# Performance work log

Hardware: AMD Instinct MI355X
Metric: run time of the kernel (lower is better)

The kernel has to match this reference:

```python
import jax, jax.numpy as jnp
import numpy as np

EPS = 1e-5


def spline_conv(x, src, dst, pseudo, W, root, bias, num_nodes, K=5):
    """Degree-1 open B-spline conv (torch_spline_conv semantics), mean aggregation.
    W: [kernel_total, Cin, Cout]. kernel_total==1 means trivial basis (kernel_size=1)."""
    E = src.shape[0]
    Cin = x.shape[1]
    KT = W.shape[0]
    x_j = x[src]                                            # [E, Cin] edge gather
    deg = jax.ops.segment_sum(jnp.ones((E,), x.dtype), dst, num_segments=num_nodes)
    deg = jnp.maximum(deg, 1.0)
    if KT == 1:
        agg = jax.ops.segment_sum(x_j, dst, num_segments=num_nodes)
        out = (agg / deg[:, None]) @ W[0]
    else:
        v = pseudo * (K - 1)                                # open spline: v in [0, K-1]
        f = jnp.clip(jnp.floor(v), 0.0, K - 2)
        frac = v - f                                        # [E, 2]
        fi = f.astype(jnp.int32)
        # bucket basis-weighted source features by (kernel_index, dst) then one dense einsum
        h = jnp.zeros((KT * num_nodes, Cin), x.dtype)
        for s0 in (0, 1):
            for s1 in (0, 1):
                b0 = frac[:, 0] if s0 else 1.0 - frac[:, 0]
                b1 = frac[:, 1] if s1 else 1.0 - frac[:, 1]
                basis = b0 * b1                             # [E]
                wi = (fi[:, 0] + s0) + K * (fi[:, 1] + s1)  # [E] kernel index in [0,25)
                seg = wi * num_nodes + dst
                h = h + jax.ops.segment_sum(basis[:, None] * x_j, seg,
                                            num_segments=KT * num_nodes)
        agg = jnp.einsum('knc,kco->no', h.reshape(KT, num_nodes, Cin), W)
        out = agg / deg[:, None]
    return out + x @ root + bias


def batch_norm(x, gamma, beta):
    m = x.mean(axis=0)
    var = jnp.mean((x - m) ** 2, axis=0)
    return gamma * (x - m) * jax.lax.rsqrt(var + EPS) + beta


def setup_inputs() -> dict:
    key = jax.random.key(0)
    ks = jax.random.split(key, 8)
    N, E, Cin, Cout = 50000, 800000, 32, 64
    x = jax.random.normal(ks[0], (N, Cin), jnp.float32)
    edge_index = jax.random.randint(ks[1], (2, E), 0, N, jnp.int32)
    edge_attr = jax.random.uniform(ks[2], (E, 2), jnp.float32)
    s = 0.1
    return {
        'x': x, 'edge_index': edge_index, 'edge_attr': edge_attr,
        'w1': jax.random.normal(ks[3], (25, Cin, Cout), jnp.float32) * s,
        'r1': jax.random.normal(ks[4], (Cin, Cout), jnp.float32) * s,
        'b1': jnp.zeros((Cout,), jnp.float32),
        'g1': jnp.ones((Cout,), jnp.float32),
        'beta1': jnp.zeros((Cout,), jnp.float32),
        'w2': jax.random.normal(ks[5], (25, Cout, Cout), jnp.float32) * s,
        'r2': jax.random.normal(ks[6], (Cout, Cout), jnp.float32) * s,
        'b2': jnp.zeros((Cout,), jnp.float32),
        'g2': jnp.ones((Cout,), jnp.float32),
        'beta2': jnp.zeros((Cout,), jnp.float32),
        'ws': jax.random.normal(ks[7], (1, Cin, Cout), jnp.float32) * s,
        'rs': jax.random.normal(jax.random.fold_in(key, 99), (Cin, Cout), jnp.float32) * s,
        'bs': jnp.zeros((Cout,), jnp.float32),
        'gs': jnp.ones((Cout,), jnp.float32),
        'betas': jnp.zeros((Cout,), jnp.float32),
    }


def reference(x, edge_index, edge_attr, w1, r1, b1, g1, beta1,
              w2, r2, b2, g2, beta2, ws, rs, bs, gs, betas):
    N = x.shape[0]
    src, dst = edge_index[0], edge_index[1]
    h = jax.nn.elu(batch_norm(spline_conv(x, src, dst, edge_attr, w1, r1, b1, N), g1, beta1))
    left = batch_norm(spline_conv(h, src, dst, edge_attr, w2, r2, b2, N), g2, beta2)
    short = batch_norm(spline_conv(x, src, dst, edge_attr, ws, rs, bs, N), gs, betas)
    return jax.nn.elu(left + short)
```

## Files before the change

kernel.cpp:

```cpp
#include <hip/hip_runtime.h>

#define NN 50000
#define NE 800000

typedef __attribute__((ext_vector_type(8))) short bf16x8;
typedef __attribute__((ext_vector_type(4))) float f32x4;
typedef __attribute__((ext_vector_type(2))) float f32x2;

__device__ __forceinline__ unsigned short f2bf(float f) {
    union { float f; unsigned u; } v; v.f = f;
    unsigned r = v.u + 0x7FFFu + ((v.u >> 16) & 1u);
    return (unsigned short)(r >> 16);
}

__device__ __forceinline__ int4 ld_ep(const int4* ep, unsigned idx) {
    return *(const int4*)((const char*)ep + (size_t)(idx * 16u));
}
__device__ __forceinline__ float ld_x(const float* X, unsigned byteoff) {
    return *(const float*)((const char*)X + (size_t)byteoff);
}

__device__ __forceinline__ int us_idx(int kk, int r, int m) {
    return kk*544 + (r >> 3)*136 + m*8 + (r & 7);
}

template<bool HS>
__device__ __forceinline__ void edge_acc(float* h, float& hs, const int4& p, float x) {
    const f32x2 zero = {0.f, 0.f};
    f32x2 vp = {__int_as_float(p.z), __int_as_float(p.w)};
    f32x2 wxy[5];
#pragma unroll
    for (int r = 0; r < 5; ++r) {
        f32x2 wr = 1.f - __builtin_elementwise_abs(vp - (float)r);
        wxy[r] = __builtin_elementwise_max(wr, zero);
    }
    if (HS) hs += x;
#pragma unroll
    for (int r1 = 0; r1 < 5; ++r1) {
        float ty = x * wxy[r1].y;
#pragma unroll
        for (int r0 = 0; r0 < 5; ++r0)
            h[r1*5 + r0] = fmaf(wxy[r0].x, ty, h[r1*5 + r0]);
    }
}

__global__ __launch_bounds__(256) void k_zero(int* degi, int* cur, float* stats) {
    int i = blockIdx.x*256 + threadIdx.x;
    int stride = gridDim.x*256;
    for (int j = i; j < NN; j += stride) { degi[j] = 0; cur[j] = 0; }
    if (i < 384) stats[i] = 0.f;
}

__global__ __launch_bounds__(256) void k_hist(const int* __restrict__ dst, int* degi) {
    int e = blockIdx.x*256 + threadIdx.x;
    if (e < NE) atomicAdd(&degi[dst[e]], 1);
}

__global__ __launch_bounds__(256) void k_scan_block(const int* __restrict__ degi,
                                                    int* off, int* bsum) {
    __shared__ int sh[256];
    int t = threadIdx.x;
    int base = blockIdx.x * 1024;
    int v[4]; int s = 0;
#pragma unroll
    for (int j = 0; j < 4; j++) {
        int idx = base + t*4 + j;
        v[j] = (idx < NN) ? degi[idx] : 0;
        s += v[j];
    }
    sh[t] = s; __syncthreads();
    for (int ofs = 1; ofs < 256; ofs <<= 1) {
        int x = (t >= ofs) ? sh[t - ofs] : 0;
        __syncthreads();
        sh[t] += x;
        __syncthreads();
    }
    int ex = sh[t] - s;
#pragma unroll
    for (int j = 0; j < 4; j++) {
        int idx = base + t*4 + j;
        if (idx < NN) off[idx] = ex;
        ex += v[j];
    }
    if (t == 255) bsum[blockIdx.x] = sh[255];
}

__global__ __launch_bounds__(256) void k_scan_top(const int* __restrict__ bsum,
                                                  int* bpre, int nb) {
    __shared__ int sh[256];
    int t = threadIdx.x;
    int s = (t < nb) ? bsum[t] : 0;
    sh[t] = s; __syncthreads();
    for (int ofs = 1; ofs < 256; ofs <<= 1) {
        int x = (t >= ofs) ? sh[t - ofs] : 0;
        __syncthreads();
        sh[t] += x;
        __syncthreads();
    }
    if (t < nb) bpre[t] = sh[t] - s;
}

__global__ __launch_bounds__(256) void k_scan_add(int* off, const int* __restrict__ bpre) {
    int i = blockIdx.x*256 + threadIdx.x;
    if (i < NN) off[i] += bpre[i >> 10];
    if (i == 0) off[NN] = NE;
}

__global__ __launch_bounds__(256) void k_scatter(const int* __restrict__ src,
                                                 const int* __restrict__ dst,
                                                 const float* __restrict__ ea,
                                                 const int* __restrict__ off, int* cur,
                                                 int4* __restrict__ ep) {
    int e = blockIdx.x*256 + threadIdx.x;
    if (e >= NE) return;
    int d = dst[e];
    int p = off[d] + atomicAdd(&cur[d], 1);
    float v0 = ea[2*e]     * 4.f;
    float v1 = ea[2*e + 1] * 4.f;
    ep[p] = make_int4(src[e], 0, __float_as_int(v0), __float_as_int(v1));
}

__global__ __launch_bounds__(256) void k_wprep(const float* __restrict__ W,
                                               const float* __restrict__ root,
                                               int KTC, unsigned short* Wb) {
    int tid = blockIdx.x*256 + threadIdx.x;
    int lane = tid & 63, cot = (tid >> 6) & 3, kk = tid >> 8;
    int co = 16*cot + (lane & 15);
    int kbase = kk*32 + ((lane >> 4) * 8);
    union { unsigned short s[8]; uint4 v; } u;
#pragma unroll
    for (int j = 0; j < 8; j++) {
        int k = kbase + j;
        float val = (k < KTC) ? W[(size_t)k*64 + co] : root[(size_t)(k - KTC)*64 + co];
        u.s[j] = f2bf(val);
    }
    *(uint4*)(Wb + (size_t)tid * 8) = u.v;
}

__global__ __launch_bounds__(512, 4) void k_conv1s(
        const float* __restrict__ X,
        const int* __restrict__ off,
        const int4* __restrict__ ep,
        const unsigned short* __restrict__ Wb1,
        const unsigned short* __restrict__ WbS,
        const float* __restrict__ b1,
        const float* __restrict__ bs,
        float* __restrict__ agg1,
        float* __restrict__ aggS) {
    __shared__ __align__(16) unsigned short hb[28*544];
    const int t = threadIdx.x;
    const int g = t >> 5;
    const int ci = t & 31;
    const int n0 = blockIdx.x * 16;
    const int n = n0 + g;

    float h[25], hs = 0.f;
#pragma unroll
    for (int i = 0; i < 25; ++i) h[i] = 0.f;

    const int ebeg = off[n], eend = off[n + 1];
    const int last = eend - 1;
    const float rdeg = 1.f / (float)max(eend - ebeg, 1);

    for (int i = ebeg; i < eend; i += 4) {
        int4 p[4]; float xv[4];
#pragma unroll
        for (int u = 0; u < 4; ++u) p[u] = ld_ep(ep, (unsigned)min(i + u, last));
#pragma unroll
        for (int u = 0; u < 4; ++u) {
            xv[u] = ld_x(X, (unsigned)p[u].x * 128u + (unsigned)ci * 4u);
            if (i + u >= eend) xv[u] = 0.f;
        }
#pragma unroll
        for (int u = 0; u < 4; ++u) edge_acc<true>(h, hs, p[u], xv[u]);
    }

    const int bw = us_idx(0, ci, g);
    const unsigned short xbf = f2bf(X[(size_t)n*32 + ci]);
#pragma unroll
    for (int wi = 0; wi < 25; ++wi) hb[wi*544 + bw] = f2bf(h[wi] * rdeg);
    hb[25*544 + bw] = xbf;
    hb[26*544 + bw] = f2bf(hs * rdeg);
    hb[27*544 + bw] = xbf;
    __syncthreads();

    const int lane = t & 63, w = t >> 6;
    const int m = lane & 15, qq = lane >> 4;
    const int co = (w & 3)*16 + m;
    if (w < 4) {
        f32x4 acc = {0.f, 0.f, 0.f, 0.f};
        for (int kk = 0; kk < 26; ++kk) {
            bf16x8 av = *(const bf16x8*)&hb[kk*544 + qq*136 + m*8];
            bf16x8 bv = *(const bf16x8*)(Wb1 + (size_t)((kk*4 + w)*64 + lane) * 8);
            acc = __builtin_amdgcn_mfma_f32_16x16x32_bf16(av, bv, acc, 0, 0, 0);
        }
        const float bb = b1[co];
#pragma unroll
        for (int r = 0; r < 4; ++r)
            agg1[(size_t)(n0 + qq*4 + r)*64 + co] = acc[r] + bb;
    } else {
        f32x4 accs = {0.f, 0.f, 0.f, 0.f};
#pragma unroll
        for (int s = 0; s < 2; ++s) {
            bf16x8 av = *(const bf16x8*)&hb[(26 + s)*544 + qq*136 + m*8];
            bf16x8 bv = *(const bf16x8*)(WbS + (size_t)((s*4 + (w & 3))*64 + lane) * 8);
            accs = __builtin_amdgcn_mfma_f32_16x16x32_bf16(av, bv, accs, 0, 0, 0);
        }
        const float bb = bs[co];
#pragma unroll
        for (int r = 0; r < 4; ++r)
            aggS[(size_t)(n0 + qq*4 + r)*64 + co] = accs[r] + bb;
    }
}

__global__ __launch_bounds__(512, 4) void k_conv2(
        const float* __restrict__ X,
        const int* __restrict__ off,
        const int4* __restrict__ ep,
        const unsigned short* __restrict__ Wb2,
        const float* __restrict__ b2,
        float* __restrict__ agg) {
    __shared__ __align__(16) unsigned short hb[52*544];
    const int t = threadIdx.x, lane = t & 63, w = t >> 6;
    const int n0 = blockIdx.x * 16;
    const int kh = lane >> 5, r = lane & 31;

#pragma unroll
    for (int nn = 0; nn < 2; ++nn) {
        const int g = 2*w + nn;
        const int n = n0 + g;
        float h[25];
#pragma unroll
        for (int i = 0; i < 25; ++i) h[i] = 0.f;
        float hsd = 0.f;

        const int ebeg = off[n], eend = off[n + 1];
        const int last = eend - 1;
        const float rdeg = 1.f / (float)max(eend - ebeg, 1);

        for (int i = ebeg; i < eend; i += 4) {
            int4 p[4]; float xv[4];
#pragma unroll
            for (int u = 0; u < 4; ++u) p[u] = ld_ep(ep, (unsigned)min(i + u, last));
#pragma unroll
            for (int u = 0; u < 4; ++u) {
                xv[u] = ld_x(X, (unsigned)p[u].x * 256u + (unsigned)lane * 4u);
                if (i + u >= eend) xv[u] = 0.f;
            }
#pragma unroll
            for (int u = 0; u < 4; ++u) edge_acc<false>(h, hsd, p[u], xv[u]);
        }

        const int bw = us_idx(0, r, g);
#pragma unroll
        for (int wi = 0; wi < 25; ++wi)
            hb[(wi*2 + kh)*544 + bw] = f2bf(h[wi] * rdeg);
        hb[(50 + kh)*544 + bw] = f2bf(X[(size_t)n*64 + lane]);
    }
    __syncthreads();

    if (w >= 4) return;

    const int m = lane & 15, qq = lane >> 4;
    f32x4 acc = {0.f, 0.f, 0.f, 0.f};
    for (int kk = 0; kk < 52; ++kk) {
        bf16x8 av = *(const bf16x8*)&hb[kk*544 + qq*136 + m*8];
        bf16x8 bv = *(const bf16x8*)(Wb2 + (size_t)((kk*4 + w)*64 + lane) * 8);
        acc = __builtin_amdgcn_mfma_f32_16x16x32_bf16(av, bv, acc, 0, 0, 0);
    }
    const int co = w*16 + m;
    const float bb = b2[co];
#pragma unroll
    for (int rr = 0; rr < 4; ++rr)
        agg[(size_t)(n0 + qq*4 + rr)*64 + co] = acc[rr] + bb;
}

__global__ __launch_bounds__(256) void k_bnstats(const float* __restrict__ agg, float* stats) {
    __shared__ float sh0[256], sh1[256];
    int t = threadIdx.x;
    float s = 0.f, ss = 0.f;
    int stride = gridDim.x * 256;
    for (int i = blockIdx.x*256 + t; i < NN*64; i += stride) {
        float v = agg[i];
        s += v; ss += v*v;
    }
    sh0[t] = s; sh1[t] = ss;
    __syncthreads();
    if (t < 64) {
        float a = sh0[t] + sh0[t+64] + sh0[t+128] + sh0[t+192];
        float b = sh1[t] + sh1[t+64] + sh1[t+128] + sh1[t+192];
        atomicAdd(&stats[t], a);
        atomicAdd(&stats[64 + t], b);
    }
}

__device__ __forceinline__ float eluf(float u) { return u > 0.f ? u : expm1f(u); }

__global__ __launch_bounds__(256) void k_bn_elu(const float* __restrict__ agg,
                                                const float* __restrict__ stats,
                                                const float* __restrict__ gamma,
                                                const float* __restrict__ beta,
                                                float* __restrict__ out) {
    int i = blockIdx.x*256 + threadIdx.x;
    if (i >= NN*16) return;
    float4 v = ((const float4*)agg)[i];
    float r[4] = {v.x, v.y, v.z, v.w};
    int c0 = (i << 2) & 63;
#pragma unroll
    for (int j = 0; j < 4; j++) {
        int c = c0 + j;
        float mu = stats[c] * (1.f/NN);
        float var = stats[64 + c] * (1.f/NN) - mu*mu;
        float sc = gamma[c] * rsqrtf(fmaxf(var, 0.f) + 1e-5f);
        r[j] = eluf((r[j] - mu)*sc + beta[c]);
    }
    ((float4*)out)[i] = make_float4(r[0], r[1], r[2], r[3]);
}

__global__ __launch_bounds__(256) void k_bn_final(const float* __restrict__ a2,
                                                  const float* __restrict__ st2,
                                                  const float* __restrict__ g2,
                                                  const float* __restrict__ be2,
                                                  const float* __restrict__ as,
                                                  const float* __restrict__ sts,
                                                  const float* __restrict__ gs,
                                                  const float* __restrict__ bes,
                                                  float* __restrict__ out) {
    int i = blockIdx.x*256 + threadIdx.x;
    if (i >= NN*16) return;
    float4 v2 = ((const float4*)a2)[i];
    float4 vs = ((const float4*)as)[i];
    float r2v[4] = {v2.x, v2.y, v2.z, v2.w};
    float rsv[4] = {vs.x, vs.y, vs.z, vs.w};
    float o[4];
    int c0 = (i << 2) & 63;
#pragma unroll
    for (int j = 0; j < 4; j++) {
        int c = c0 + j;
        float mu2 = st2[c] * (1.f/NN);
        float var2 = st2[64 + c] * (1.f/NN) - mu2*mu2;
        float sc2 = g2[c] * rsqrtf(fmaxf(var2, 0.f) + 1e-5f);
        float mus = sts[c] * (1.f/NN);
        float vars = sts[64 + c] * (1.f/NN) - mus*mus;
        float scs = gs[c] * rsqrtf(fmaxf(vars, 0.f) + 1e-5f);
        float u = (r2v[j] - mu2)*sc2 + be2[c] + (rsv[j] - mus)*scs + bes[c];
        o[j] = eluf(u);
    }
    ((float4*)out)[i] = make_float4(o[0], o[1], o[2], o[3]);
}

extern "C" void kernel_launch(void* const* d_in, const int* in_sizes, int n_in,
                              void* d_out, int out_size, void* d_ws, size_t ws_size,
                              hipStream_t stream) {
    const float* x   = (const float*)d_in[0];
    const int*   ei  = (const int*)d_in[1];
    const float* ea  = (const float*)d_in[2];
    const float* w1  = (const float*)d_in[3];
    const float* r1  = (const float*)d_in[4];
    const float* b1  = (const float*)d_in[5];
    const float* g1  = (const float*)d_in[6];
    const float* be1 = (const float*)d_in[7];
    const float* w2  = (const float*)d_in[8];
    const float* r2  = (const float*)d_in[9];
    const float* b2  = (const float*)d_in[10];
    const float* g2  = (const float*)d_in[11];
    const float* be2 = (const float*)d_in[12];
    const float* wsN = (const float*)d_in[13];
    const float* rs  = (const float*)d_in[14];
    const float* bs  = (const float*)d_in[15];
    const float* gs  = (const float*)d_in[16];
    const float* bes = (const float*)d_in[17];
    const int* srcp = ei;
    const int* dstp = ei + NE;

    char* wsb = (char*)d_ws;
    size_t o = 0;
    auto alloc = [&](size_t bytes) -> char* {
        char* p = wsb + o;
        o += (bytes + 255) & ~(size_t)255;
        return p;
    };
    int*    degi    = (int*)   alloc((size_t)NN * 4);
    int*    cur     = (int*)   alloc((size_t)NN * 4);
    int*    off     = (int*)   alloc((size_t)(NN + 1) * 4);
    int*    bsum    = (int*)   alloc(256 * 4);
    int*    bpre    = (int*)   alloc(256 * 4);
    int4*   ep      = (int4*)  alloc((size_t)NE * 16);
    unsigned short* Wb1 = (unsigned short*)alloc(26 * 4096);
    unsigned short* WbS = (unsigned short*)alloc(2 * 4096);
    unsigned short* Wb2 = (unsigned short*)alloc(52 * 4096);
    float*  agg1    = (float*) alloc((size_t)NN * 64 * 4);
    float*  aggS    = (float*) alloc((size_t)NN * 64 * 4);
    float*  h1      = (float*) alloc((size_t)NN * 64 * 4);
    float*  stats   = (float*) alloc(384 * 4);
    (void)ws_size; (void)in_sizes; (void)n_in; (void)out_size;

    float* out = (float*)d_out;

    k_zero<<<196, 256, 0, stream>>>(degi, cur, stats);
    k_hist<<<3125, 256, 0, stream>>>(dstp, degi);
    k_scan_block<<<49, 256, 0, stream>>>(degi, off, bsum);
    k_scan_top<<<1, 256, 0, stream>>>(bsum, bpre, 49);
    k_scan_add<<<196, 256, 0, stream>>>(off, bpre);
    k_scatter<<<3125, 256, 0, stream>>>(srcp, dstp, ea, off, cur, ep);

    k_wprep<<<26, 256, 0, stream>>>(w1, r1, 800, Wb1);
    k_wprep<<<2, 256, 0, stream>>>(wsN, rs, 32, WbS);
    k_wprep<<<52, 256, 0, stream>>>(w2, r2, 1600, Wb2);

    k_conv1s<<<3125, 512, 0, stream>>>(x, off, ep, Wb1, WbS, b1, bs, agg1, aggS);
    k_bnstats<<<256, 256, 0, stream>>>(agg1, stats);
    k_bn_elu<<<3125, 256, 0, stream>>>(agg1, stats, g1, be1, h1);

    k_conv2<<<3125, 512, 0, stream>>>(h1, off, ep, Wb2, b2, agg1);
    k_bnstats<<<256, 256, 0, stream>>>(agg1, stats + 128);
    k_bnstats<<<256, 256, 0, stream>>>(aggS, stats + 256);
    k_bn_final<<<3125, 256, 0, stream>>>(agg1, stats + 128, g2, be2,
                                         aggS, stats + 256, gs, bes, out);
}
```

Before: 481.5 us.

## Pad CSR segments to multiples of four and split conv2 LDS staging

Each node's edge segment is padded to a multiple of four, filled with dummy entries that point to an appended zero row in x and h1. This removes the per-edge clamp and mask from the gather loops. Edge records now store byte offsets precomputed for both feature widths, so the index multiply is gone. conv2 halves its shared-memory buffer by staging the 26 k-slices in two rounds with an extra MFMA pass and sync, which may raise occupancy. The cost is an extra copy of x, a pad-fill kernel, more edge-record traffic, and more registers for holding two nodes' accumulators.

```diff
diff --git a/kernel.cpp b/kernel.cpp
--- a/kernel.cpp
+++ b/kernel.cpp
@@ -2,6 +2,7 @@
 
 #define NN 50000
 #define NE 800000
+#define NEP (NE + 4*NN)
 
 typedef __attribute__((ext_vector_type(8))) short bf16x8;
 typedef __attribute__((ext_vector_type(4))) float f32x4;
@@ -13,8 +14,8 @@
     return (unsigned short)(r >> 16);
 }
 
-__device__ __forceinline__ int4 ld_ep(const int4* ep, unsigned idx) {
-    return *(const int4*)((const char*)ep + (size_t)(idx * 16u));
+__device__ __forceinline__ int4 ld_ep(const int4* ep, unsigned byteoff) {
+    return *(const int4*)((const char*)ep + (size_t)byteoff);
 }
 __device__ __forceinline__ float ld_x(const float* X, unsigned byteoff) {
     return *(const float*)((const char*)X + (size_t)byteoff);
@@ -65,7 +66,7 @@
 #pragma unroll
     for (int j = 0; j < 4; j++) {
         int idx = base + t*4 + j;
-        v[j] = (idx < NN) ? degi[idx] : 0;
+        v[j] = (idx < NN) ? ((degi[idx] + 3) & ~3) : 0;
         s += v[j];
     }
     sh[t] = s; __syncthreads();
@@ -103,7 +104,6 @@
 __global__ __launch_bounds__(256) void k_scan_add(int* off, const int* __restrict__ bpre) {
     int i = blockIdx.x*256 + threadIdx.x;
     if (i < NN) off[i] += bpre[i >> 10];
-    if (i == 0) off[NN] = NE;
 }
 
 __global__ __launch_bounds__(256) void k_scatter(const int* __restrict__ src,
@@ -117,7 +117,26 @@
     int p = off[d] + atomicAdd(&cur[d], 1);
     float v0 = ea[2*e]     * 4.f;
     float v1 = ea[2*e + 1] * 4.f;
-    ep[p] = make_int4(src[e], 0, __float_as_int(v0), __float_as_int(v1));
+    int s = src[e];
+    ep[p] = make_int4(s*256, s*128, __float_as_int(v0), __float_as_int(v1));
+}
+
+__global__ __launch_bounds__(256) void k_padfill(const int* __restrict__ degi,
+                                                 const int* __restrict__ off,
+                                                 int4* __restrict__ ep) {
+    int n = blockIdx.x*256 + threadIdx.x;
+    if (n >= NN) return;
+    int d = degi[n];
+    int pd = (d + 3) & ~3;
+    int4 dummy = make_int4(NN*256, NN*128, 0, 0);
+    int base = off[n];
+    for (int j = d; j < pd; ++j) ep[base + j] = dummy;
+}
+
+__global__ __launch_bounds__(256) void k_xz(const float4* __restrict__ x4, float4* xz4) {
+    int i = blockIdx.x*256 + threadIdx.x;
+    if (i < NN*8) xz4[i] = x4[i];
+    else if (i < NN*8 + 8) xz4[i] = make_float4(0.f, 0.f, 0.f, 0.f);
 }
 
 __global__ __launch_bounds__(256) void k_wprep(const float* __restrict__ W,
@@ -138,8 +157,9 @@
 }
 
 __global__ __launch_bounds__(512, 4) void k_conv1s(
-        const float* __restrict__ X,
+        const float* __restrict__ XZ,
         const int* __restrict__ off,
+        const int* __restrict__ degi,
         const int4* __restrict__ ep,
         const unsigned short* __restrict__ Wb1,
         const unsigned short* __restrict__ WbS,
@@ -151,6 +171,7 @@
     const int t = threadIdx.x;
     const int g = t >> 5;
     const int ci = t & 31;
+    const unsigned ci4 = (unsigned)ci * 4u;
     const int n0 = blockIdx.x * 16;
     const int n = n0 + g;
 
@@ -158,25 +179,23 @@
 #pragma unroll
     for (int i = 0; i < 25; ++i) h[i] = 0.f;
 
-    const int ebeg = off[n], eend = off[n + 1];
-    const int last = eend - 1;
-    const float rdeg = 1.f / (float)max(eend - ebeg, 1);
-
-    for (int i = ebeg; i < eend; i += 4) {
+    const int d = degi[n];
+    const float rdeg = 1.f / (float)max(d, 1);
+    unsigned b = (unsigned)off[n] * 16u;
+    const unsigned bend = b + (unsigned)((d + 3) & ~3) * 16u;
+
+    for (; b < bend; b += 64u) {
         int4 p[4]; float xv[4];
 #pragma unroll
-        for (int u = 0; u < 4; ++u) p[u] = ld_ep(ep, (unsigned)min(i + u, last));
-#pragma unroll
-        for (int u = 0; u < 4; ++u) {
-            xv[u] = ld_x(X, (unsigned)p[u].x * 128u + (unsigned)ci * 4u);
-            if (i + u >= eend) xv[u] = 0.f;
-        }
+        for (int u = 0; u < 4; ++u) p[u] = ld_ep(ep, b + u*16u);
+#pragma unroll
+        for (int u = 0; u < 4; ++u) xv[u] = ld_x(XZ, (unsigned)p[u].y + ci4);
 #pragma unroll
         for (int u = 0; u < 4; ++u) edge_acc<true>(h, hs, p[u], xv[u]);
     }
 
     const int bw = us_idx(0, ci, g);
-    const unsigned short xbf = f2bf(X[(size_t)n*32 + ci]);
+    const unsigned short xbf = f2bf(XZ[(size_t)n*32 + ci]);
 #pragma unroll
     for (int wi = 0; wi < 25; ++wi) hb[wi*544 + bw] = f2bf(h[wi] * rdeg);
     hb[25*544 + bw] = xbf;
@@ -214,58 +233,74 @@
 }
 
 __global__ __launch_bounds__(512, 4) void k_conv2(
-        const float* __restrict__ X,
+        const float* __restrict__ XZ,
         const int* __restrict__ off,
+        const int* __restrict__ degi,
         const int4* __restrict__ ep,
         const unsigned short* __restrict__ Wb2,
         const float* __restrict__ b2,
         float* __restrict__ agg) {
-    __shared__ __align__(16) unsigned short hb[52*544];
+    __shared__ __align__(16) unsigned short hb[26*544];
     const int t = threadIdx.x, lane = t & 63, w = t >> 6;
     const int n0 = blockIdx.x * 16;
     const int kh = lane >> 5, r = lane & 31;
-
+    const unsigned l4 = (unsigned)lane * 4u;
+
+    float h[2][25];
+    float rdg[2];
 #pragma unroll
     for (int nn = 0; nn < 2; ++nn) {
-        const int g = 2*w + nn;
-        const int n = n0 + g;
-        float h[25];
-#pragma unroll
-        for (int i = 0; i < 25; ++i) h[i] = 0.f;
+        const int n = n0 + 2*w + nn;
+#pragma unroll
+        for (int i = 0; i < 25; ++i) h[nn][i] = 0.f;
         float hsd = 0.f;
-
-        const int ebeg = off[n], eend = off[n + 1];
-        const int last = eend - 1;
-        const float rdeg = 1.f / (float)max(eend - ebeg, 1);
-
-        for (int i = ebeg; i < eend; i += 4) {
+        const int d = degi[n];
+        rdg[nn] = 1.f / (float)max(d, 1);
+        unsigned b = (unsigned)off[n] * 16u;
+        const unsigned bend = b + (unsigned)((d + 3) & ~3) * 16u;
+        for (; b < bend; b += 64u) {
             int4 p[4]; float xv[4];
 #pragma unroll
-            for (int u = 0; u < 4; ++u) p[u] = ld_ep(ep, (unsigned)min(i + u, last));
-#pragma unroll
-            for (int u = 0; u < 4; ++u) {
-                xv[u] = ld_x(X, (unsigned)p[u].x * 256u + (unsigned)lane * 4u);
-                if (i + u >= eend) xv[u] = 0.f;
-            }
-#pragma unroll
-            for (int u = 0; u < 4; ++u) edge_acc<false>(h, hsd, p[u], xv[u]);
+            for (int u = 0; u < 4; ++u) p[u] = ld_ep(ep, b + u*16u);
+#pragma unroll
+            for (int u = 0; u < 4; ++u) xv[u] = ld_x(XZ, (unsigned)p[u].x + l4);
+#pragma unroll
+            for (int u = 0; u < 4; ++u) edge_acc<false>(h[nn], hsd, p[u], xv[u]);
         }
-
-        const int bw = us_idx(0, r, g);
-#pragma unroll
-        for (int wi = 0; wi < 25; ++wi)
-            hb[(wi*2 + kh)*544 + bw] = f2bf(h[wi] * rdeg);
-        hb[(50 + kh)*544 + bw] = f2bf(X[(size_t)n*64 + lane]);
+    }
+
+    const int m = lane & 15, qq = lane >> 4;
+    const int bwA = us_idx(0, r, 2*w), bwB = us_idx(0, r, 2*w + 1);
+    f32x4 acc = {0.f, 0.f, 0.f, 0.f};
+
+#pragma unroll
+    for (int wi = 0; wi < 13; ++wi) {
+        hb[(wi*2 + kh)*544 + bwA] = f2bf(h[0][wi] * rdg[0]);
+        hb[(wi*2 + kh)*544 + bwB] = f2bf(h[1][wi] * rdg[1]);
     }
     __syncthreads();
+    if (w < 4) {
+        for (int kk = 0; kk < 26; ++kk) {
+            bf16x8 av = *(const bf16x8*)&hb[kk*544 + qq*136 + m*8];
+            bf16x8 bv = *(const bf16x8*)(Wb2 + (size_t)((kk*4 + w)*64 + lane) * 8);
+            acc = __builtin_amdgcn_mfma_f32_16x16x32_bf16(av, bv, acc, 0, 0, 0);
+        }
+    }
+    __syncthreads();
+
+#pragma unroll
+    for (int wi = 13; wi < 25; ++wi) {
+        hb[((wi - 13)*2 + kh)*544 + bwA] = f2bf(h[0][wi] * rdg[0]);
+        hb[((wi - 13)*2 + kh)*544 + bwB] = f2bf(h[1][wi] * rdg[1]);
+    }
+    hb[(24 + kh)*544 + bwA] = f2bf(XZ[(size_t)(n0 + 2*w)*64 + lane]);
+    hb[(24 + kh)*544 + bwB] = f2bf(XZ[(size_t)(n0 + 2*w + 1)*64 + lane]);
+    __syncthreads();
 
     if (w >= 4) return;
-
-    const int m = lane & 15, qq = lane >> 4;
-    f32x4 acc = {0.f, 0.f, 0.f, 0.f};
-    for (int kk = 0; kk < 52; ++kk) {
+    for (int kk = 0; kk < 26; ++kk) {
         bf16x8 av = *(const bf16x8*)&hb[kk*544 + qq*136 + m*8];
-        bf16x8 bv = *(const bf16x8*)(Wb2 + (size_t)((kk*4 + w)*64 + lane) * 8);
+        bf16x8 bv = *(const bf16x8*)(Wb2 + (size_t)(((26 + kk)*4 + w)*64 + lane) * 8);
         acc = __builtin_amdgcn_mfma_f32_16x16x32_bf16(av, bv, acc, 0, 0, 0);
     }
     const int co = w*16 + m;
@@ -302,7 +337,10 @@
                                                 const float* __restrict__ beta,
                                                 float* __restrict__ out) {
     int i = blockIdx.x*256 + threadIdx.x;
-    if (i >= NN*16) return;
+    if (i >= NN*16) {
+        if (i < NN*16 + 16) ((float4*)out)[i] = make_float4(0.f, 0.f, 0.f, 0.f);
+        return;
+    }
     float4 v = ((const float4*)agg)[i];
     float r[4] = {v.x, v.y, v.z, v.w};
     int c0 = (i << 2) & 63;
@@ -385,13 +423,14 @@
     int*    off     = (int*)   alloc((size_t)(NN + 1) * 4);
     int*    bsum    = (int*)   alloc(256 * 4);
     int*    bpre    = (int*)   alloc(256 * 4);
-    int4*   ep      = (int4*)  alloc((size_t)NE * 16);
+    int4*   ep      = (int4*)  alloc((size_t)NEP * 16);
     unsigned short* Wb1 = (unsigned short*)alloc(26 * 4096);
     unsigned short* WbS = (unsigned short*)alloc(2 * 4096);
     unsigned short* Wb2 = (unsigned short*)alloc(52 * 4096);
+    float*  xz      = (float*) alloc((size_t)(NN + 1) * 32 * 4);
     float*  agg1    = (float*) alloc((size_t)NN * 64 * 4);
     float*  aggS    = (float*) alloc((size_t)NN * 64 * 4);
-    float*  h1      = (float*) alloc((size_t)NN * 64 * 4);
+    float*  h1      = (float*) alloc((size_t)(NN + 1) * 64 * 4);
     float*  stats   = (float*) alloc(384 * 4);
     (void)ws_size; (void)in_sizes; (void)n_in; (void)out_size;
 
@@ -403,16 +442,18 @@
     k_scan_top<<<1, 256, 0, stream>>>(bsum, bpre, 49);
     k_scan_add<<<196, 256, 0, stream>>>(off, bpre);
     k_scatter<<<3125, 256, 0, stream>>>(srcp, dstp, ea, off, cur, ep);
+    k_padfill<<<196, 256, 0, stream>>>(degi, off, ep);
+    k_xz<<<1564, 256, 0, stream>>>((const float4*)x, (float4*)xz);
 
     k_wprep<<<26, 256, 0, stream>>>(w1, r1, 800, Wb1);
     k_wprep<<<2, 256, 0, stream>>>(wsN, rs, 32, WbS);
     k_wprep<<<52, 256, 0, stream>>>(w2, r2, 1600, Wb2);
 
-    k_conv1s<<<3125, 512, 0, stream>>>(x, off, ep, Wb1, WbS, b1, bs, agg1, aggS);
+    k_conv1s<<<3125, 512, 0, stream>>>(xz, off, degi, ep, Wb1, WbS, b1, bs, agg1, aggS);
     k_bnstats<<<256, 256, 0, stream>>>(agg1, stats);
-    k_bn_elu<<<3125, 256, 0, stream>>>(agg1, stats, g1, be1, h1);
-
-    k_conv2<<<3125, 512, 0, stream>>>(h1, off, ep, Wb2, b2, agg1);
+    k_bn_elu<<<3126, 256, 0, stream>>>(agg1, stats, g1, be1, h1);
+
+    k_conv2<<<3125, 512, 0, stream>>>(h1, off, degi, ep, Wb2, b2, agg1);
     k_bnstats<<<256, 256, 0, stream>>>(agg1, stats + 128);
     k_bnstats<<<256, 256, 0, stream>>>(aggS, stats + 256);
     k_bn_final<<<3125, 256, 0, stream>>>(agg1, stats + 128, g2, be2,
```

Measured after the change: 483.8 us. Within noise of the previous version (+0.5%).
